# Kernel tuning notes

Measured on AMD Instinct MI355X. Metric: run time of the kernel, lower is better.

The kernel has to match this reference:

```python
import jax, jax.numpy as jnp
import numpy as np

D_MODEL = 1024
D_STATE = 16
D_CONV = 4
D_INNER = 2 * D_MODEL
DT_RANK = 64
BATCH = 2
SEQ = 1024
EPS = 1e-6


def setup_inputs() -> dict:
    key = jax.random.key(0)
    ks = jax.random.split(key, 8)
    s = 0.02
    return {
        "x": jax.random.normal(ks[0], (BATCH, SEQ, D_MODEL), jnp.float32),
        "norm_w": jnp.ones((D_MODEL,), jnp.float32),
        "in_proj_w": jax.random.normal(ks[1], (2 * D_INNER, D_MODEL), jnp.float32) * s,
        "conv_w": jax.random.normal(ks[2], (D_INNER, 1, D_CONV), jnp.float32) * s,
        "conv_b": jnp.zeros((D_INNER,), jnp.float32),
        "x_proj_w": jax.random.normal(ks[3], (DT_RANK + 2 * D_STATE, D_INNER), jnp.float32) * s,
        "dt_proj_w": jax.random.normal(ks[4], (D_INNER, DT_RANK), jnp.float32) * s,
        "dt_proj_b": jnp.zeros((D_INNER,), jnp.float32),
        "A_log": jnp.tile(jnp.log(jnp.arange(1, D_STATE + 1, dtype=jnp.float32)), (D_INNER, 1)),
        "D_diag": jnp.ones((D_INNER,), jnp.float32),
        "out_proj_w": jax.random.normal(ks[5], (D_MODEL, D_INNER), jnp.float32) * s,
    }


def reference(x, norm_w, in_proj_w, conv_w, conv_b, x_proj_w, dt_proj_w, dt_proj_b, A_log, D_diag, out_proj_w):
    residual = x
    # RMSNorm
    ms = jnp.mean(x * x, axis=-1, keepdims=True)
    xn = x * jax.lax.rsqrt(ms + EPS) * norm_w
    # in_proj -> split into x branch and gate z
    xz = xn @ in_proj_w.T  # [B, L, 2*d_inner]
    xc, z = jnp.split(xz, 2, axis=-1)
    # depthwise causal conv1d with padding d_conv-1, truncated to L
    xc = xc.transpose(0, 2, 1)  # [B, d_inner, L]
    conv = jax.lax.conv_general_dilated(
        xc, conv_w, window_strides=(1,), padding=[(D_CONV - 1, D_CONV - 1)],
        feature_group_count=D_INNER, dimension_numbers=("NCH", "OIH", "NCH"))
    conv = conv[:, :, :SEQ] + conv_b[None, :, None]
    u = jax.nn.silu(conv.transpose(0, 2, 1))  # [B, L, d_inner]
    # input-dependent dt, B, C
    proj = u @ x_proj_w.T  # [B, L, dt_rank + 2*d_state]
    dt_raw = proj[..., :DT_RANK]
    b_raw = proj[..., DT_RANK:DT_RANK + D_STATE]
    c_raw = proj[..., DT_RANK + D_STATE:]
    dt = jax.nn.softplus(dt_raw @ dt_proj_w.T + dt_proj_b)  # [B, L, d_inner]
    A = -jnp.exp(A_log)  # [d_inner, d_state]

    def step(state, inp):
        dt_t, u_t, b_t, c_t = inp  # [B,d], [B,d], [B,n], [B,n]
        dA = jnp.exp(dt_t[:, :, None] * A)  # [B, d, n]
        state = dA * state + dt_t[:, :, None] * b_t[:, None, :] * u_t[:, :, None]
        y_t = jnp.einsum("bdn,bn->bd", state, c_t) + D_diag * u_t
        return state, y_t

    xs = (dt.transpose(1, 0, 2), u.transpose(1, 0, 2),
          b_raw.transpose(1, 0, 2), c_raw.transpose(1, 0, 2))
    state0 = jnp.zeros((x.shape[0], D_INNER, D_STATE), x.dtype)
    _, ys = jax.lax.scan(step, state0, xs)  # ys: [L, B, d_inner]
    y = ys.transpose(1, 0, 2)
    y = y * jax.nn.silu(z)
    y = y @ out_proj_w.T
    return residual + y
```

## Files before the change

### kernel.cpp

```cpp
#include <hip/hip_runtime.h>
#include <hip/hip_bf16.h>
#include <math.h>

#define D_MODEL 1024
#define D_STATE 16
#define D_CONV 4
#define D_INNER 2048
#define DT_RANK 64
#define BATCH 2
#define SEQ 1024
#define NTOK (BATCH * SEQ)
#define XPROJ_N (DT_RANK + 2 * D_STATE)
#define EPS 1e-6f

#define NCHUNK 32
#define CHLEN (SEQ / NCHUNK)

#define XK_SPLIT 16
#define OK_SPLIT 2

typedef __attribute__((ext_vector_type(8))) short bf16x8;
typedef __attribute__((ext_vector_type(4))) float f32x4;
typedef __hip_bfloat16 bf16;

__device__ inline void gload_lds16(const void* g, void* l) {
  __builtin_amdgcn_global_load_lds(
      (const __attribute__((address_space(1))) void*)g,
      (__attribute__((address_space(3))) void*)l, 16, 0, 0);
}

__device__ inline unsigned short f2bfu(float f) {
  bf16 h = __float2bfloat16(f);
  return *(unsigned short*)&h;
}

__device__ inline float bfu2f(short s) {
  bf16 h;
  *(short*)&h = s;
  return __bfloat162float(h);
}

#define WS0 (4096 * 1024)
#define WS1 (96 * 2048)
#define WS2 (2048 * 64)
#define WS3 (1024 * 2048)
__global__ __launch_bounds__(256) void f2bf_all_kernel(
    const float* __restrict__ w0, bf16* __restrict__ o0,
    const float* __restrict__ w1, bf16* __restrict__ o1,
    const float* __restrict__ w2, bf16* __restrict__ o2,
    const float* __restrict__ w3, bf16* __restrict__ o3) {
  int base = (blockIdx.x * 256 + threadIdx.x) * 4;
  const float* in;
  bf16* out;
  int off;
  if (base < WS0) {
    in = w0; out = o0; off = base;
  } else if (base < WS0 + WS1) {
    in = w1; out = o1; off = base - WS0;
  } else if (base < WS0 + WS1 + WS2) {
    in = w2; out = o2; off = base - WS0 - WS1;
  } else {
    in = w3; out = o3; off = base - WS0 - WS1 - WS2;
  }
  float4 v = *(const float4*)(in + off);
  ushort4 o;
  o.x = f2bfu(v.x); o.y = f2bfu(v.y); o.z = f2bfu(v.z); o.w = f2bfu(v.w);
  *(ushort4*)(out + off) = o;
}

__global__ __launch_bounds__(256) void rmsnorm_kernel(
    const float* __restrict__ x, const float* __restrict__ w,
    bf16* __restrict__ xn) {
  int token = blockIdx.x;
  int tid = threadIdx.x;
  const float* xr = x + (size_t)token * D_MODEL;
  float v[4];
  float s = 0.f;
#pragma unroll
  for (int i = 0; i < 4; ++i) {
    v[i] = xr[tid + i * 256];
    s += v[i] * v[i];
  }
#pragma unroll
  for (int off = 32; off > 0; off >>= 1) s += __shfl_down(s, off, 64);
  __shared__ float warp_s[4];
  if ((tid & 63) == 0) warp_s[tid >> 6] = s;
  __syncthreads();
  float total = warp_s[0] + warp_s[1] + warp_s[2] + warp_s[3];
  float scale = rsqrtf(total / (float)D_MODEL + EPS);
  bf16* xo = xn + (size_t)token * D_MODEL;
#pragma unroll
  for (int i = 0; i < 4; ++i)
    xo[tid + i * 256] = __float2bfloat16(v[i] * scale * w[tid + i * 256]);
}

template <int EPI, int BN>
__global__ __launch_bounds__(256) void gemm_bf16(
    const bf16* __restrict__ A, int lda, const bf16* __restrict__ B, int ldb,
    bf16* __restrict__ C, int ldc, int M, int N, int K,
    const float* __restrict__ bias) {
  constexpr int NJ = BN / 32;
  __shared__ bf16 As[2][128 * 32];
  __shared__ bf16 Bs[2][BN * 32];
  const int tid = threadIdx.x;
  const int lane = tid & 63;
  const int wave = tid >> 6;
  const int wm = wave >> 1;
  const int wn = wave & 1;
  const int bm = blockIdx.y;
  const int bn = blockIdx.x;

  f32x4 acc[4][NJ] = {};

  const int kchunk = K / (int)gridDim.z;
  const int kb = blockIdx.z * kchunk;
  const int kend = kb + kchunk;

  const int lrow = lane & 15;
  const int lk = (lane >> 4) * 8;

  auto stage = [&](int buf, int k0) {
#pragma unroll
    for (int r = 0; r < 2; ++r) {
      int idx = r * 256 + tid;
      gload_lds16(A + (size_t)(bm * 128 + (idx >> 2)) * lda + k0 + (idx & 3) * 8,
                  &As[buf][idx * 8]);
    }
#pragma unroll
    for (int r = 0; r < BN / 64; ++r) {
      int idx = r * 256 + tid;
      gload_lds16(B + (size_t)(bn * BN + (idx >> 2)) * ldb + k0 + (idx & 3) * 8,
                  &Bs[buf][idx * 8]);
    }
  };

  stage(0, kb);
  asm volatile("s_waitcnt vmcnt(0)\ns_barrier" ::: "memory");

  int cur = 0;
  for (int k0 = kb; k0 < kend; k0 += 32) {
    if (k0 + 32 < kend) stage(cur ^ 1, k0 + 32);

    bf16x8 a[4], b[NJ];
#pragma unroll
    for (int i = 0; i < 4; ++i)
      a[i] = *(const bf16x8*)(&As[cur][(wm * 64 + i * 16 + lrow) * 32 + lk]);
#pragma unroll
    for (int j = 0; j < NJ; ++j)
      b[j] = *(const bf16x8*)(&Bs[cur][(wn * (BN / 2) + j * 16 + lrow) * 32 + lk]);
#pragma unroll
    for (int i = 0; i < 4; ++i)
#pragma unroll
      for (int j = 0; j < NJ; ++j)
        acc[i][j] =
            __builtin_amdgcn_mfma_f32_16x16x32_bf16(a[i], b[j], acc[i][j], 0, 0, 0);

    asm volatile("s_waitcnt vmcnt(0)\ns_barrier" ::: "memory");
    cur ^= 1;
  }

#pragma unroll
  for (int j = 0; j < NJ; ++j) {
    int col = bn * BN + wn * (BN / 2) + j * 16 + lrow;
    if (col < N) {
      float bv = (EPI == 1) ? bias[col] : 0.f;
#pragma unroll
      for (int i = 0; i < 4; ++i) {
#pragma unroll
        for (int reg = 0; reg < 4; ++reg) {
          int row = bm * 128 + wm * 64 + i * 16 + (lane >> 4) * 4 + reg;
          float v = acc[i][j][reg];
          if (EPI == 1) {
            v += bv;
            v = (v > 20.f) ? v : log1pf(__expf(v));
          }
          size_t off;
          if (EPI == 3) {
            off = ((size_t)blockIdx.z * M + row) * ldc + col;
          } else {
            off = (size_t)row * ldc + col;
          }
          C[off] = __float2bfloat16(v);
        }
      }
    }
  }
}

__global__ __launch_bounds__(256) void reduce_proj_kernel(
    const bf16* __restrict__ part, float* __restrict__ proj,
    bf16* __restrict__ projbf) {
  int i = blockIdx.x * 256 + threadIdx.x;
  float s = 0.f;
#pragma unroll
  for (int z = 0; z < XK_SPLIT; ++z)
    s += __bfloat162float(part[(size_t)z * NTOK * XPROJ_N + i]);
  proj[i] = s;
  projbf[i] = __float2bfloat16(s);
}

__global__ __launch_bounds__(256) void reduce_out_kernel(
    const bf16* __restrict__ part, const float* __restrict__ resid,
    float* __restrict__ out) {
  int i = (blockIdx.x * 256 + threadIdx.x) * 8;
  bf16x8 p0 = *(const bf16x8*)(part + i);
  bf16x8 p1 = *(const bf16x8*)(part + (size_t)NTOK * D_MODEL + i);
  float4 r0 = *(const float4*)(resid + i);
  float4 r1 = *(const float4*)(resid + i + 4);
  float4 o0, o1;
  o0.x = bfu2f(p0[0]) + bfu2f(p1[0]) + r0.x;
  o0.y = bfu2f(p0[1]) + bfu2f(p1[1]) + r0.y;
  o0.z = bfu2f(p0[2]) + bfu2f(p1[2]) + r0.z;
  o0.w = bfu2f(p0[3]) + bfu2f(p1[3]) + r0.w;
  o1.x = bfu2f(p0[4]) + bfu2f(p1[4]) + r1.x;
  o1.y = bfu2f(p0[5]) + bfu2f(p1[5]) + r1.y;
  o1.z = bfu2f(p0[6]) + bfu2f(p1[6]) + r1.z;
  o1.w = bfu2f(p0[7]) + bfu2f(p1[7]) + r1.w;
  *(float4*)(out + i) = o0;
  *(float4*)(out + i + 4) = o1;
}

__global__ __launch_bounds__(256) void conv_silu_kernel(
    const bf16* __restrict__ xz, const float* __restrict__ cw,
    const float* __restrict__ cb, bf16* __restrict__ u) {
  int id = blockIdx.x * 256 + threadIdx.x;
  int c8 = id & 255;
  int token = id >> 8;
  int d0 = c8 * 8;
  int t = token & (SEQ - 1);

  float acc[8];
  {
    float4 b0 = *(const float4*)(cb + d0);
    float4 b1 = *(const float4*)(cb + d0 + 4);
    acc[0] = b0.x; acc[1] = b0.y; acc[2] = b0.z; acc[3] = b0.w;
    acc[4] = b1.x; acc[5] = b1.y; acc[6] = b1.z; acc[7] = b1.w;
  }
  float4 wv[8];
#pragma unroll
  for (int k = 0; k < 8; ++k) wv[k] = *(const float4*)(cw + (d0 + k) * 4);

#pragma unroll
  for (int j = 0; j < D_CONV; ++j) {
    int tt = t - (D_CONV - 1) + j;
    if (tt >= 0) {
      bf16x8 v = *(const bf16x8*)(xz + (size_t)(token - (D_CONV - 1) + j) * 4096 + d0);
#pragma unroll
      for (int k = 0; k < 8; ++k)
        acc[k] = fmaf(((const float*)&wv[k])[j], bfu2f(v[k]), acc[k]);
    }
  }

  bf16x8 o;
#pragma unroll
  for (int k = 0; k < 8; ++k) {
    float s = acc[k] / (1.f + __expf(-acc[k]));
    o[k] = (short)f2bfu(s);
  }
  *(bf16x8*)(u + (size_t)token * D_INNER + d0) = o;
}

__global__ __launch_bounds__(256) void scan_pass1(
    const float* __restrict__ proj, const bf16* __restrict__ dtb,
    const bf16* __restrict__ u, const float* __restrict__ A_log,
    bf16* __restrict__ s_end, bf16* __restrict__ decay) {
  int tid = threadIdx.x;
  int d = blockIdx.x * 256 + tid;
  int c = blockIdx.y;
  int b = blockIdx.z;
  size_t tok0 = (size_t)b * SEQ + (size_t)c * CHLEN;

  __shared__ float Bs[CHLEN][D_STATE];
  for (int i = tid; i < CHLEN * D_STATE; i += 256) {
    int t = i >> 4, n = i & 15;
    Bs[t][n] = proj[(tok0 + t) * XPROJ_N + DT_RANK + n];
  }
  __syncthreads();

  float An[16], st[16];
#pragma unroll
  for (int n = 0; n < 16; ++n) {
    An[n] = -__expf(A_log[d * D_STATE + n]);
    st[n] = 0.f;
  }
  float dtsum = 0.f;

  for (int t = 0; t < CHLEN; ++t) {
    float dtv = __bfloat162float(dtb[(tok0 + t) * D_INNER + d]);
    float uv = __bfloat162float(u[(tok0 + t) * D_INNER + d]);
    float dtu = dtv * uv;
    dtsum += dtv;
#pragma unroll
    for (int n = 0; n < 16; ++n)
      st[n] = fmaf(__expf(An[n] * dtv), st[n], dtu * Bs[t][n]);
  }

  size_t base = (((size_t)b * NCHUNK + c) * D_INNER + d) * D_STATE;
#pragma unroll
  for (int n = 0; n < 16; ++n) {
    s_end[base + n] = __float2bfloat16(st[n]);
    decay[base + n] = __float2bfloat16(__expf(An[n] * dtsum));
  }
}

__global__ __launch_bounds__(256) void scan_pass2(
    const bf16* __restrict__ s_end, const bf16* __restrict__ decay,
    bf16* __restrict__ s0) {
  int gid = blockIdx.x * 256 + threadIdx.x;
  int b = gid >> 15;
  int dn = gid & (D_INNER * D_STATE - 1);
  float s = 0.f;
  for (int c = 0; c < NCHUNK; ++c) {
    size_t idx = ((size_t)(b * NCHUNK + c) * D_INNER * D_STATE) + dn;
    s0[idx] = __float2bfloat16(s);
    s = fmaf(__bfloat162float(decay[idx]), s, __bfloat162float(s_end[idx]));
  }
}

__global__ __launch_bounds__(256) void scan_pass3(
    const float* __restrict__ proj, const bf16* __restrict__ dtb,
    const bf16* __restrict__ u, const bf16* __restrict__ xz,
    const float* __restrict__ A_log, const float* __restrict__ D_diag,
    const bf16* __restrict__ s0, bf16* __restrict__ y) {
  int tid = threadIdx.x;
  int d = blockIdx.x * 256 + tid;
  int c = blockIdx.y;
  int b = blockIdx.z;
  size_t tok0 = (size_t)b * SEQ + (size_t)c * CHLEN;

  __shared__ float BC[CHLEN][2 * D_STATE];
  for (int i = tid; i < CHLEN * 2 * D_STATE; i += 256) {
    int t = i >> 5, col = i & 31;
    BC[t][col] = proj[(tok0 + t) * XPROJ_N + DT_RANK + col];
  }
  __syncthreads();

  float An[16], st[16];
  size_t base = (((size_t)b * NCHUNK + c) * D_INNER + d) * D_STATE;
#pragma unroll
  for (int n = 0; n < 16; ++n) {
    An[n] = -__expf(A_log[d * D_STATE + n]);
    st[n] = __bfloat162float(s0[base + n]);
  }
  float Dd = D_diag[d];

  for (int t = 0; t < CHLEN; ++t) {
    size_t tok = tok0 + t;
    float dtv = __bfloat162float(dtb[tok * D_INNER + d]);
    float uv = __bfloat162float(u[tok * D_INNER + d]);
    float zv = __bfloat162float(xz[tok * (2 * D_INNER) + D_INNER + d]);
    float dtu = dtv * uv;
    float yv = Dd * uv;
#pragma unroll
    for (int n = 0; n < 16; ++n) {
      st[n] = fmaf(__expf(An[n] * dtv), st[n], dtu * BC[t][n]);
      yv = fmaf(st[n], BC[t][D_STATE + n], yv);
    }
    y[tok * D_INNER + d] = __float2bfloat16(yv * (zv / (1.f + __expf(-zv))));
  }
}

extern "C" void kernel_launch(void* const* d_in, const int* in_sizes, int n_in,
                              void* d_out, int out_size, void* d_ws,
                              size_t ws_size, hipStream_t stream) {
  const float* x         = (const float*)d_in[0];
  const float* norm_w    = (const float*)d_in[1];
  const float* in_proj_w = (const float*)d_in[2];
  const float* conv_w    = (const float*)d_in[3];
  const float* conv_b    = (const float*)d_in[4];
  const float* x_proj_w  = (const float*)d_in[5];
  const float* dt_proj_w = (const float*)d_in[6];
  const float* dt_proj_b = (const float*)d_in[7];
  const float* A_log     = (const float*)d_in[8];
  const float* D_diag    = (const float*)d_in[9];
  const float* out_proj_w= (const float*)d_in[10];
  float* out = (float*)d_out;

  char* p = (char*)d_ws;
  bf16* xz    = (bf16*)p;  p += (size_t)NTOK * 4096 * 2;
  bf16* dt    = (bf16*)p;  p += (size_t)NTOK * D_INNER * 2;
  float* proj = (float*)p; p += (size_t)NTOK * XPROJ_N * 4;
  bf16* projbf= (bf16*)p;  p += (size_t)NTOK * XPROJ_N * 2;
  bf16* u_bf  = (bf16*)p;  p += (size_t)NTOK * D_INNER * 2;
  bf16* ybuf  = (bf16*)p;  p += (size_t)NTOK * D_INNER * 2;
  bf16* in_w  = (bf16*)p;  p += (size_t)4096 * 1024 * 2;
  bf16* xw    = (bf16*)p;  p += (size_t)128 * 2048 * 2;
  bf16* dtw   = (bf16*)p;  p += (size_t)2048 * 64 * 2;
  bf16* ow    = (bf16*)p;  p += (size_t)1024 * 2048 * 2;
  char* un = p;
  const size_t AGGB = (size_t)BATCH * NCHUNK * D_INNER * D_STATE * 2;
  bf16* ppart = (bf16*)un;
  bf16* xn_bf = (bf16*)(un + (size_t)XK_SPLIT * NTOK * XPROJ_N * 2);
  bf16* s_end = (bf16*)un;
  bf16* decay = (bf16*)(un + AGGB);
  bf16* s0    = (bf16*)(un + 2 * AGGB);
  bf16* opart = (bf16*)(un + 3 * AGGB);

  {
    int total = WS0 + WS1 + WS2 + WS3;
    f2bf_all_kernel<<<total / 1024, 256, 0, stream>>>(
        in_proj_w, in_w, x_proj_w, xw, dt_proj_w, dtw, out_proj_w, ow);
  }

  rmsnorm_kernel<<<NTOK, 256, 0, stream>>>(x, norm_w, xn_bf);

  {
    dim3 grid(4096 / 64, NTOK / 128, 1);
    gemm_bf16<0, 64><<<grid, 256, 0, stream>>>(xn_bf, D_MODEL, in_w, D_MODEL,
                                               xz, 2 * D_INNER, NTOK,
                                               2 * D_INNER, D_MODEL, nullptr);
  }

  conv_silu_kernel<<<NTOK, 256, 0, stream>>>(xz, conv_w, conv_b, u_bf);

  {
    dim3 grid(1, NTOK / 128, XK_SPLIT);
    gemm_bf16<3, 128><<<grid, 256, 0, stream>>>(u_bf, D_INNER, xw, D_INNER,
                                                ppart, XPROJ_N, NTOK, XPROJ_N,
                                                D_INNER, nullptr);
    reduce_proj_kernel<<<NTOK * XPROJ_N / 256, 256, 0, stream>>>(ppart, proj,
                                                                 projbf);
  }

  {
    dim3 grid(D_INNER / 64, NTOK / 128, 1);
    gemm_bf16<1, 64><<<grid, 256, 0, stream>>>(projbf, XPROJ_N, dtw, DT_RANK,
                                               dt, D_INNER, NTOK, D_INNER,
                                               DT_RANK, dt_proj_b);
  }

  {
    dim3 grid(D_INNER / 256, NCHUNK, BATCH);
    scan_pass1<<<grid, 256, 0, stream>>>(proj, dt, u_bf, A_log, s_end, decay);
    scan_pass2<<<BATCH * D_INNER * D_STATE / 256, 256, 0, stream>>>(s_end,
                                                                    decay, s0);
    scan_pass3<<<grid, 256, 0, stream>>>(proj, dt, u_bf, xz, A_log, D_diag, s0,
                                         ybuf);
  }

  {
    dim3 grid(D_MODEL / 64, NTOK / 128, OK_SPLIT);
    gemm_bf16<3, 64><<<grid, 256, 0, stream>>>(ybuf, D_INNER, ow, D_INNER,
                                               opart, D_MODEL, NTOK, D_MODEL,
                                               D_INNER, nullptr);
    reduce_out_kernel<<<NTOK * D_MODEL / 2048, 256, 0, stream>>>(opart, x, out);
  }
}
```

Measured before the change: 170.0 us.

## Retile GEMMs with swizzled LDS, fuse prologue kernels and residual epilogue

Merges the weight-conversion and RMSNorm kernels into a single prologue launch. The GEMM template is parameterised over BM/BN/BK, uses BK=64 with an XOR-swizzled LDS layout to cut bank conflicts, and moves to 64-row tiles so more blocks are launched. The out-projection drops its split-K partials and separate reduce kernel and instead adds the residual and writes fp32 output directly in the GEMM epilogue. This saves launches and intermediate traffic, but leaves fewer K-parallel blocks for the out-projection and gives smaller tiles less reuse.

```diff
diff --git a/kernel.cpp b/kernel.cpp
--- a/kernel.cpp
+++ b/kernel.cpp
@@ -17,7 +17,6 @@
 #define CHLEN (SEQ / NCHUNK)
 
 #define XK_SPLIT 16
-#define OK_SPLIT 2
 
 typedef __attribute__((ext_vector_type(8))) short bf16x8;
 typedef __attribute__((ext_vector_type(4))) float f32x4;
@@ -44,64 +43,69 @@
 #define WS1 (96 * 2048)
 #define WS2 (2048 * 64)
 #define WS3 (1024 * 2048)
-__global__ __launch_bounds__(256) void f2bf_all_kernel(
+#define NWCONV ((WS0 + WS1 + WS2 + WS3) / 1024)
+__global__ __launch_bounds__(256) void prologue_kernel(
+    const float* __restrict__ x, const float* __restrict__ nw,
+    bf16* __restrict__ xn,
     const float* __restrict__ w0, bf16* __restrict__ o0,
     const float* __restrict__ w1, bf16* __restrict__ o1,
     const float* __restrict__ w2, bf16* __restrict__ o2,
     const float* __restrict__ w3, bf16* __restrict__ o3) {
-  int base = (blockIdx.x * 256 + threadIdx.x) * 4;
-  const float* in;
-  bf16* out;
-  int off;
-  if (base < WS0) {
-    in = w0; out = o0; off = base;
-  } else if (base < WS0 + WS1) {
-    in = w1; out = o1; off = base - WS0;
-  } else if (base < WS0 + WS1 + WS2) {
-    in = w2; out = o2; off = base - WS0 - WS1;
+  int tid = threadIdx.x;
+  if (blockIdx.x < NTOK) {
+    int token = blockIdx.x;
+    const float* xr = x + (size_t)token * D_MODEL;
+    float v[4];
+    float s = 0.f;
+#pragma unroll
+    for (int i = 0; i < 4; ++i) {
+      v[i] = xr[tid + i * 256];
+      s += v[i] * v[i];
+    }
+#pragma unroll
+    for (int off = 32; off > 0; off >>= 1) s += __shfl_down(s, off, 64);
+    __shared__ float warp_s[4];
+    if ((tid & 63) == 0) warp_s[tid >> 6] = s;
+    __syncthreads();
+    float total = warp_s[0] + warp_s[1] + warp_s[2] + warp_s[3];
+    float scale = rsqrtf(total / (float)D_MODEL + EPS);
+    bf16* xo = xn + (size_t)token * D_MODEL;
+#pragma unroll
+    for (int i = 0; i < 4; ++i)
+      xo[tid + i * 256] = __float2bfloat16(v[i] * scale * nw[tid + i * 256]);
   } else {
-    in = w3; out = o3; off = base - WS0 - WS1 - WS2;
-  }
-  float4 v = *(const float4*)(in + off);
-  ushort4 o;
-  o.x = f2bfu(v.x); o.y = f2bfu(v.y); o.z = f2bfu(v.z); o.w = f2bfu(v.w);
-  *(ushort4*)(out + off) = o;
-}
-
-__global__ __launch_bounds__(256) void rmsnorm_kernel(
-    const float* __restrict__ x, const float* __restrict__ w,
-    bf16* __restrict__ xn) {
-  int token = blockIdx.x;
-  int tid = threadIdx.x;
-  const float* xr = x + (size_t)token * D_MODEL;
-  float v[4];
-  float s = 0.f;
-#pragma unroll
-  for (int i = 0; i < 4; ++i) {
-    v[i] = xr[tid + i * 256];
-    s += v[i] * v[i];
-  }
-#pragma unroll
-  for (int off = 32; off > 0; off >>= 1) s += __shfl_down(s, off, 64);
-  __shared__ float warp_s[4];
-  if ((tid & 63) == 0) warp_s[tid >> 6] = s;
-  __syncthreads();
-  float total = warp_s[0] + warp_s[1] + warp_s[2] + warp_s[3];
-  float scale = rsqrtf(total / (float)D_MODEL + EPS);
-  bf16* xo = xn + (size_t)token * D_MODEL;
-#pragma unroll
-  for (int i = 0; i < 4; ++i)
-    xo[tid + i * 256] = __float2bfloat16(v[i] * scale * w[tid + i * 256]);
-}
-
-template <int EPI, int BN>
+    int base = ((blockIdx.x - NTOK) * 256 + tid) * 4;
+    const float* in;
+    bf16* out;
+    int off;
+    if (base < WS0) {
+      in = w0; out = o0; off = base;
+    } else if (base < WS0 + WS1) {
+      in = w1; out = o1; off = base - WS0;
+    } else if (base < WS0 + WS1 + WS2) {
+      in = w2; out = o2; off = base - WS0 - WS1;
+    } else {
+      in = w3; out = o3; off = base - WS0 - WS1 - WS2;
+    }
+    float4 v = *(const float4*)(in + off);
+    ushort4 o;
+    o.x = f2bfu(v.x); o.y = f2bfu(v.y); o.z = f2bfu(v.z); o.w = f2bfu(v.w);
+    *(ushort4*)(out + off) = o;
+  }
+}
+
+template <int EPI, int BM, int BN, int BK>
 __global__ __launch_bounds__(256) void gemm_bf16(
     const bf16* __restrict__ A, int lda, const bf16* __restrict__ B, int ldb,
     bf16* __restrict__ C, int ldc, int M, int N, int K,
-    const float* __restrict__ bias) {
+    const float* __restrict__ bias, const float* __restrict__ resid) {
+  constexpr int AI = BM / 32;
   constexpr int NJ = BN / 32;
-  __shared__ bf16 As[2][128 * 32];
-  __shared__ bf16 Bs[2][BN * 32];
+  constexpr int KV = BK / 8;
+  constexpr int AL = BM * BK / 2048;
+  constexpr int BL = BN * BK / 2048;
+  __shared__ bf16 As[2][BM * BK];
+  __shared__ bf16 Bs[2][BN * BK];
   const int tid = threadIdx.x;
   const int lane = tid & 63;
   const int wave = tid >> 6;
@@ -110,7 +114,7 @@
   const int bm = blockIdx.y;
   const int bn = blockIdx.x;
 
-  f32x4 acc[4][NJ] = {};
+  f32x4 acc[AI][NJ] = {};
 
   const int kchunk = K / (int)gridDim.z;
   const int kb = blockIdx.z * kchunk;
@@ -121,15 +125,21 @@
 
   auto stage = [&](int buf, int k0) {
 #pragma unroll
-    for (int r = 0; r < 2; ++r) {
+    for (int r = 0; r < AL; ++r) {
       int idx = r * 256 + tid;
-      gload_lds16(A + (size_t)(bm * 128 + (idx >> 2)) * lda + k0 + (idx & 3) * 8,
+      int row = idx / KV;
+      int kc = (idx % KV) * 8;
+      int kcs = kc ^ ((row & 7) * 8);
+      gload_lds16(A + (size_t)(bm * BM + row) * lda + k0 + kcs,
                   &As[buf][idx * 8]);
     }
 #pragma unroll
-    for (int r = 0; r < BN / 64; ++r) {
+    for (int r = 0; r < BL; ++r) {
       int idx = r * 256 + tid;
-      gload_lds16(B + (size_t)(bn * BN + (idx >> 2)) * ldb + k0 + (idx & 3) * 8,
+      int row = idx / KV;
+      int kc = (idx % KV) * 8;
+      int kcs = kc ^ ((row & 7) * 8);
+      gload_lds16(B + (size_t)(bn * BN + row) * ldb + k0 + kcs,
                   &Bs[buf][idx * 8]);
     }
   };
@@ -138,22 +148,31 @@
   asm volatile("s_waitcnt vmcnt(0)\ns_barrier" ::: "memory");
 
   int cur = 0;
-  for (int k0 = kb; k0 < kend; k0 += 32) {
-    if (k0 + 32 < kend) stage(cur ^ 1, k0 + 32);
-
-    bf16x8 a[4], b[NJ];
-#pragma unroll
-    for (int i = 0; i < 4; ++i)
-      a[i] = *(const bf16x8*)(&As[cur][(wm * 64 + i * 16 + lrow) * 32 + lk]);
-#pragma unroll
-    for (int j = 0; j < NJ; ++j)
-      b[j] = *(const bf16x8*)(&Bs[cur][(wn * (BN / 2) + j * 16 + lrow) * 32 + lk]);
-#pragma unroll
-    for (int i = 0; i < 4; ++i)
-#pragma unroll
-      for (int j = 0; j < NJ; ++j)
-        acc[i][j] =
-            __builtin_amdgcn_mfma_f32_16x16x32_bf16(a[i], b[j], acc[i][j], 0, 0, 0);
+  for (int k0 = kb; k0 < kend; k0 += BK) {
+    if (k0 + BK < kend) stage(cur ^ 1, k0 + BK);
+
+#pragma unroll
+    for (int ks = 0; ks < BK / 32; ++ks) {
+      bf16x8 a[AI], b[NJ];
+#pragma unroll
+      for (int i = 0; i < AI; ++i) {
+        int row = wm * (BM / 2) + i * 16 + lrow;
+        a[i] = *(const bf16x8*)(
+            &As[cur][row * BK + ((ks * 32 + lk) ^ ((row & 7) * 8))]);
+      }
+#pragma unroll
+      for (int j = 0; j < NJ; ++j) {
+        int row = wn * (BN / 2) + j * 16 + lrow;
+        b[j] = *(const bf16x8*)(
+            &Bs[cur][row * BK + ((ks * 32 + lk) ^ ((row & 7) * 8))]);
+      }
+#pragma unroll
+      for (int i = 0; i < AI; ++i)
+#pragma unroll
+        for (int j = 0; j < NJ; ++j)
+          acc[i][j] = __builtin_amdgcn_mfma_f32_16x16x32_bf16(a[i], b[j],
+                                                              acc[i][j], 0, 0, 0);
+    }
 
     asm volatile("s_waitcnt vmcnt(0)\ns_barrier" ::: "memory");
     cur ^= 1;
@@ -165,22 +184,23 @@
     if (col < N) {
       float bv = (EPI == 1) ? bias[col] : 0.f;
 #pragma unroll
-      for (int i = 0; i < 4; ++i) {
+      for (int i = 0; i < AI; ++i) {
 #pragma unroll
         for (int reg = 0; reg < 4; ++reg) {
-          int row = bm * 128 + wm * 64 + i * 16 + (lane >> 4) * 4 + reg;
+          int row = bm * BM + wm * (BM / 2) + i * 16 + (lane >> 4) * 4 + reg;
           float v = acc[i][j][reg];
           if (EPI == 1) {
             v += bv;
             v = (v > 20.f) ? v : log1pf(__expf(v));
           }
-          size_t off;
-          if (EPI == 3) {
-            off = ((size_t)blockIdx.z * M + row) * ldc + col;
+          if (EPI == 2) {
+            ((float*)C)[(size_t)row * ldc + col] =
+                v + resid[(size_t)row * ldc + col];
+          } else if (EPI == 3) {
+            C[((size_t)blockIdx.z * M + row) * ldc + col] = __float2bfloat16(v);
           } else {
-            off = (size_t)row * ldc + col;
+            C[(size_t)row * ldc + col] = __float2bfloat16(v);
           }
-          C[off] = __float2bfloat16(v);
         }
       }
     }
@@ -197,27 +217,6 @@
     s += __bfloat162float(part[(size_t)z * NTOK * XPROJ_N + i]);
   proj[i] = s;
   projbf[i] = __float2bfloat16(s);
-}
-
-__global__ __launch_bounds__(256) void reduce_out_kernel(
-    const bf16* __restrict__ part, const float* __restrict__ resid,
-    float* __restrict__ out) {
-  int i = (blockIdx.x * 256 + threadIdx.x) * 8;
-  bf16x8 p0 = *(const bf16x8*)(part + i);
-  bf16x8 p1 = *(const bf16x8*)(part + (size_t)NTOK * D_MODEL + i);
-  float4 r0 = *(const float4*)(resid + i);
-  float4 r1 = *(const float4*)(resid + i + 4);
-  float4 o0, o1;
-  o0.x = bfu2f(p0[0]) + bfu2f(p1[0]) + r0.x;
-  o0.y = bfu2f(p0[1]) + bfu2f(p1[1]) + r0.y;
-  o0.z = bfu2f(p0[2]) + bfu2f(p1[2]) + r0.z;
-  o0.w = bfu2f(p0[3]) + bfu2f(p1[3]) + r0.w;
-  o1.x = bfu2f(p0[4]) + bfu2f(p1[4]) + r1.x;
-  o1.y = bfu2f(p0[5]) + bfu2f(p1[5]) + r1.y;
-  o1.z = bfu2f(p0[6]) + bfu2f(p1[6]) + r1.z;
-  o1.w = bfu2f(p0[7]) + bfu2f(p1[7]) + r1.w;
-  *(float4*)(out + i) = o0;
-  *(float4*)(out + i + 4) = o1;
 }
 
 __global__ __launch_bounds__(256) void conv_silu_kernel(
@@ -394,39 +393,34 @@
   bf16* s_end = (bf16*)un;
   bf16* decay = (bf16*)(un + AGGB);
   bf16* s0    = (bf16*)(un + 2 * AGGB);
-  bf16* opart = (bf16*)(un + 3 * AGGB);
-
-  {
-    int total = WS0 + WS1 + WS2 + WS3;
-    f2bf_all_kernel<<<total / 1024, 256, 0, stream>>>(
-        in_proj_w, in_w, x_proj_w, xw, dt_proj_w, dtw, out_proj_w, ow);
-  }
-
-  rmsnorm_kernel<<<NTOK, 256, 0, stream>>>(x, norm_w, xn_bf);
-
-  {
-    dim3 grid(4096 / 64, NTOK / 128, 1);
-    gemm_bf16<0, 64><<<grid, 256, 0, stream>>>(xn_bf, D_MODEL, in_w, D_MODEL,
-                                               xz, 2 * D_INNER, NTOK,
-                                               2 * D_INNER, D_MODEL, nullptr);
+
+  prologue_kernel<<<NTOK + NWCONV, 256, 0, stream>>>(
+      x, norm_w, xn_bf, in_proj_w, in_w, x_proj_w, xw, dt_proj_w, dtw,
+      out_proj_w, ow);
+
+  {
+    dim3 grid(4096 / 64, NTOK / 64, 1);
+    gemm_bf16<0, 64, 64, 64><<<grid, 256, 0, stream>>>(
+        xn_bf, D_MODEL, in_w, D_MODEL, xz, 2 * D_INNER, NTOK, 2 * D_INNER,
+        D_MODEL, nullptr, nullptr);
   }
 
   conv_silu_kernel<<<NTOK, 256, 0, stream>>>(xz, conv_w, conv_b, u_bf);
 
   {
-    dim3 grid(1, NTOK / 128, XK_SPLIT);
-    gemm_bf16<3, 128><<<grid, 256, 0, stream>>>(u_bf, D_INNER, xw, D_INNER,
-                                                ppart, XPROJ_N, NTOK, XPROJ_N,
-                                                D_INNER, nullptr);
+    dim3 grid(1, NTOK / 64, XK_SPLIT);
+    gemm_bf16<3, 64, 128, 64><<<grid, 256, 0, stream>>>(
+        u_bf, D_INNER, xw, D_INNER, ppart, XPROJ_N, NTOK, XPROJ_N, D_INNER,
+        nullptr, nullptr);
     reduce_proj_kernel<<<NTOK * XPROJ_N / 256, 256, 0, stream>>>(ppart, proj,
                                                                  projbf);
   }
 
   {
-    dim3 grid(D_INNER / 64, NTOK / 128, 1);
-    gemm_bf16<1, 64><<<grid, 256, 0, stream>>>(projbf, XPROJ_N, dtw, DT_RANK,
-                                               dt, D_INNER, NTOK, D_INNER,
-                                               DT_RANK, dt_proj_b);
+    dim3 grid(D_INNER / 64, NTOK / 64, 1);
+    gemm_bf16<1, 64, 64, 64><<<grid, 256, 0, stream>>>(
+        projbf, XPROJ_N, dtw, DT_RANK, dt, D_INNER, NTOK, D_INNER, DT_RANK,
+        dt_proj_b, nullptr);
   }
 
   {
@@ -439,10 +433,9 @@
   }
 
   {
-    dim3 grid(D_MODEL / 64, NTOK / 128, OK_SPLIT);
-    gemm_bf16<3, 64><<<grid, 256, 0, stream>>>(ybuf, D_INNER, ow, D_INNER,
-                                               opart, D_MODEL, NTOK, D_MODEL,
-                                               D_INNER, nullptr);
-    reduce_out_kernel<<<NTOK * D_MODEL / 2048, 256, 0, stream>>>(opart, x, out);
-  }
-}
+    dim3 grid(D_MODEL / 64, NTOK / 64, 1);
+    gemm_bf16<2, 64, 64, 64><<<grid, 256, 0, stream>>>(
+        ybuf, D_INNER, ow, D_INNER, (bf16*)out, D_MODEL, NTOK, D_MODEL,
+        D_INNER, nullptr, x);
+  }
+}
```

Result: faster. 160.2 us (-5.7%).
